# Optimization experiments

Measured on AMD Instinct MI355X. Metric: run time of the kernel, lower is better.

The kernel has to match this reference:

```python
import jax, jax.numpy as jnp
import numpy as np

L, B, S, D, H, E = 3, 2, 2048, 1024, 16, 4
Dh = D // H  # 64
DF = E * D   # 4096


def _ln(x, g, b, eps=1e-5):
    m = jnp.mean(x, axis=-1, keepdims=True)
    v = jnp.mean(jnp.square(x - m), axis=-1, keepdims=True)
    return (x - m) * jax.lax.rsqrt(v + eps) * g + b


def setup_inputs() -> dict:
    key = jax.random.key(0)
    ks = jax.random.split(key, 12)
    s = 0.02
    f32 = jnp.float32
    return {
        "x":    jax.random.normal(ks[0], (B, S, D), f32),
        "Wq":   jax.random.normal(ks[1], (L, Dh, Dh), f32) * s,
        "Wk":   jax.random.normal(ks[2], (L, Dh, Dh), f32) * s,
        "Wv":   jax.random.normal(ks[3], (L, Dh, Dh), f32) * s,
        "Wo":   jax.random.normal(ks[4], (L, D, D), f32) * s,
        "bo":   jnp.zeros((L, D), f32),
        "ln1_g": jnp.ones((L, D), f32),
        "ln1_b": jnp.zeros((L, D), f32),
        "W1":   jax.random.normal(ks[5], (L, DF, D), f32) * s,
        "b1":   jnp.zeros((L, DF), f32),
        "W2":   jax.random.normal(ks[6], (L, D, DF), f32) * s,
        "b2":   jnp.zeros((L, D), f32),
        "ln2_g": jnp.ones((L, D), f32),
        "ln2_b": jnp.zeros((L, D), f32),
    }


def reference(x, Wq, Wk, Wv, Wo, bo, ln1_g, ln1_b, W1, b1, W2, b2, ln2_g, ln2_b):
    scale = 1.0 / np.sqrt(Dh).astype(np.float32)
    out = x
    for l in range(L):
        xh = out.reshape(B, S, H, Dh)
        # per-head Linear (shared 64x64 weight across heads), torch Linear: y = x @ W.T
        q = jnp.einsum('bshd,ed->bhse', xh, Wq[l])  # [B,H,S,Dh]
        k = jnp.einsum('bshd,ed->bhse', xh, Wk[l])
        v = jnp.einsum('bshd,ed->bhse', xh, Wv[l])
        att = jax.nn.softmax(jnp.einsum('bhse,bhte->bhst', q, k) * scale, axis=-1)
        ctx = jnp.einsum('bhst,bhtd->bshd', att, v).reshape(B, S, D)
        att_out = ctx @ Wo[l].T + bo[l]
        n1 = _ln(att_out + out, ln1_g[l], ln1_b[l])  # residual adds layer input (v == out)
        ff = jax.nn.relu(n1 @ W1[l].T + b1[l]) @ W2[l].T + b2[l]
        out = _ln(ff + n1, ln2_g[l], ln2_b[l])
    return out
```

## Files before the change

kernel.cpp:

```cpp
#include <hip/hip_runtime.h>
#include <hip/hip_bf16.h>
#include <math.h>


#define DEVINL __device__ __forceinline__
typedef unsigned short ushort_t;
using short8 = __attribute__((ext_vector_type(8))) short;
using f32x4  = __attribute__((ext_vector_type(4))) float;

#if defined(__has_builtin)
#if __has_builtin(__builtin_amdgcn_exp2f)
#define EXPFN(x) __builtin_amdgcn_exp2f(x)
#define QSCALE 0.18033688011112042f
#define HAVE_EXP2 1
#endif
#endif
#ifndef HAVE_EXP2
#define EXPFN(x) __expf(x)
#define QSCALE 0.125f
#endif

DEVINL short f2b(float f) {
  unsigned u = __float_as_uint(f);
  u += 0x7fff + ((u >> 16) & 1);
  return (short)(u >> 16);
}
DEVINL unsigned pk2(float a, float b) {
  unsigned ua = __float_as_uint(a), ub = __float_as_uint(b);
  ua += 0x7fff + ((ua >> 16) & 1);
  ub += 0x7fff + ((ub >> 16) & 1);
  return (ua >> 16) | (ub & 0xffff0000u);
}
DEVINL unsigned pkc(float a, float b) {
  float2 f; f.x = a; f.y = b;
  __hip_bfloat162 h = __float22bfloat162_rn(f);
  return *reinterpret_cast<unsigned*>(&h);
}
DEVINL float bl(unsigned u) { return __uint_as_float(u << 16); }
DEVINL float bh(unsigned u) { return __uint_as_float(u & 0xffff0000u); }
DEVINL f32x4 mfma16(short8 a, short8 b, f32x4 c) {
  return __builtin_amdgcn_mfma_f32_16x16x32_bf16(a, b, c, 0, 0, 0);
}

typedef __attribute__((address_space(3))) void lds_void;
typedef __attribute__((address_space(1))) void gbl_void;
DEVINL void gl16(const void* g, void* l) {
  __builtin_amdgcn_global_load_lds((const gbl_void*)(unsigned long long)g,
                                   (lds_void*)(unsigned long long)l, 16, 0, 0);
}
template <int N> DEVINL void waitvm() {
  asm volatile("s_waitcnt vmcnt(%0)" ::"n"(N) : "memory");
}
DEVINL void barrier_raw() { __builtin_amdgcn_s_barrier(); }
DEVINL void sched0() { __builtin_amdgcn_sched_barrier(0); }

__global__ __launch_bounds__(256)
void conv_bf16(const float* __restrict__ src, ushort_t* __restrict__ dst,
               int n8) {
  int i = blockIdx.x * 256 + threadIdx.x;
  const int stride = gridDim.x * 256;
  for (; i < n8; i += stride) {
    float4 a = ((const float4*)src)[2 * i];
    float4 b = ((const float4*)src)[2 * i + 1];
    uint4 o;
    o.x = pk2(a.x, a.y); o.y = pk2(a.z, a.w);
    o.z = pk2(b.x, b.y); o.w = pk2(b.z, b.w);
    ((uint4*)dst)[i] = o;
  }
}

DEVINL float block_sum(float v, float* red) {
#pragma unroll
  for (int off = 32; off > 0; off >>= 1) v += __shfl_xor(v, off, 64);
  if ((threadIdx.x & 63) == 0) red[threadIdx.x >> 6] = v;
  __syncthreads();
  float r = red[0] + red[1] + red[2] + red[3];
  __syncthreads();
  return r;
}

template <bool WF>
__global__ __launch_bounds__(256)
void ln_fuse(const ushort_t* __restrict__ pa, const ushort_t* __restrict__ pb,
             const float* __restrict__ bias, const ushort_t* __restrict__ Rb,
             const float* __restrict__ g, const float* __restrict__ b,
             ushort_t* __restrict__ outb, float* __restrict__ outf) {
  __shared__ float red[4];
  const size_t base = (size_t)blockIdx.x * 1024 + threadIdx.x * 4;
  uint2 ua = *(const uint2*)(pa + base);
  uint2 ub = *(const uint2*)(pb + base);
  uint2 ur = *(const uint2*)(Rb + base);
  float4 vbi = *(const float4*)(bias + threadIdx.x * 4);
  float4 v;
  v.x = bl(ua.x) + bl(ub.x) + bl(ur.x) + vbi.x;
  v.y = bh(ua.x) + bh(ub.x) + bh(ur.x) + vbi.y;
  v.z = bl(ua.y) + bl(ub.y) + bl(ur.y) + vbi.z;
  v.w = bh(ua.y) + bh(ub.y) + bh(ur.y) + vbi.w;
  float s = block_sum(v.x + v.y + v.z + v.w, red);
  float mean = s * (1.0f / 1024.0f);
  float dx = v.x - mean, dy = v.y - mean, dz = v.z - mean, dw = v.w - mean;
  float sq = block_sum(dx * dx + dy * dy + dz * dz + dw * dw, red);
  float rstd = rsqrtf(sq * (1.0f / 1024.0f) + 1e-5f);
  const float4 gv = *(const float4*)(g + threadIdx.x * 4);
  const float4 bv = *(const float4*)(b + threadIdx.x * 4);
  float4 o;
  o.x = dx * rstd * gv.x + bv.x;
  o.y = dy * rstd * gv.y + bv.y;
  o.z = dz * rstd * gv.z + bv.z;
  o.w = dw * rstd * gv.w + bv.w;
  uint2 p;
  p.x = pk2(o.x, o.y); p.y = pk2(o.z, o.w);
  *(uint2*)(outb + base) = p;
  if (WF) *(float4*)(outf + base) = o;
}

template <int BM, int BN, int WR, int WC, bool OBF, int EPI, bool SWZ>
__global__ __launch_bounds__(WR * WC * 64)
void gemm_db(const ushort_t* __restrict__ A, const ushort_t* __restrict__ W,
             const float* __restrict__ bias, void* __restrict__ Cp, int M,
             int N, int Klen, int lda, int ldw) {
  constexpr int THREADS = WR * WC * 64;
  constexpr int FM = BM / WR / 16;
  constexpr int FN = BN / WC / 16;
  constexpr int CA = BM * 8 / THREADS;
  constexpr int CB = BN * 8 / THREADS;
  constexpr int L = CA + CB;
  __shared__ __align__(16) ushort_t As[2][BM * 64];
  __shared__ __align__(16) ushort_t Bs[2][BN * 64];
  const int tid = threadIdx.x;
  const int lane = tid & 63, lo = lane & 15, hi = lane >> 4, w = tid >> 6;
  int bx = blockIdx.x, by = blockIdx.y;
  if (SWZ) {
    int id = by * gridDim.x + bx;
    const int cpx = (gridDim.x * gridDim.y) >> 3;
    id = (id & 7) * cpx + (id >> 3);
    bx = id % gridDim.x;
    by = id / gridDim.x;
  }
  const int m0 = by * BM, n0 = bx * BN;
  const int wm = (w / WC) * (BM / WR), wn = (w % WC) * (BN / WC);
  const int kbase = blockIdx.z * Klen;

  auto stage = [&](int t, int buf) {
    const int k0 = kbase + t * 64;
#pragma unroll
    for (int i = 0; i < CA; ++i) {
      const int c = i * THREADS + tid;
      const int r = c >> 3, sg = (c & 7) ^ (r & 7);
      gl16(A + (size_t)(m0 + r) * lda + k0 + sg * 8, &As[buf][c * 8]);
    }
#pragma unroll
    for (int i = 0; i < CB; ++i) {
      const int c = i * THREADS + tid;
      const int r = c >> 3, sg = (c & 7) ^ (r & 7);
      gl16(W + (size_t)(n0 + r) * ldw + k0 + sg * 8, &Bs[buf][c * 8]);
    }
  };

  f32x4 acc[FM][FN] = {};
  auto compute = [&](int cur) {
#pragma unroll
    for (int ks = 0; ks < 2; ++ks) {
      short8 af[FM], bf_[FN];
#pragma unroll
      for (int fm = 0; fm < FM; ++fm) {
        const int row = wm + fm * 16 + lo;
        af[fm] = *(const short8*)
            &As[cur][row * 64 + (((ks * 4 + hi) ^ (row & 7)) << 3)];
      }
#pragma unroll
      for (int fn = 0; fn < FN; ++fn) {
        const int row = wn + fn * 16 + lo;
        bf_[fn] = *(const short8*)
            &Bs[cur][row * 64 + (((ks * 4 + hi) ^ (row & 7)) << 3)];
      }
#pragma unroll
      for (int fm = 0; fm < FM; ++fm)
#pragma unroll
        for (int fn = 0; fn < FN; ++fn)
          acc[fm][fn] = mfma16(af[fm], bf_[fn], acc[fm][fn]);
    }
  };

  const int nt = Klen / 64;
  stage(0, 0);
  for (int t = 0; t < nt - 1; ++t) {
    const int cur = t & 1;
    stage(t + 1, cur ^ 1);
    waitvm<L>();
    barrier_raw(); sched0();
    compute(cur);
    barrier_raw(); sched0();
  }
  waitvm<0>();
  barrier_raw(); sched0();
  compute((nt - 1) & 1);

  float bv[FN];
#pragma unroll
  for (int fn = 0; fn < FN; ++fn)
    bv[fn] = (EPI & 1) ? bias[n0 + wn + fn * 16 + lo] : 0.f;
#pragma unroll
  for (int fm = 0; fm < FM; ++fm)
#pragma unroll
    for (int fn = 0; fn < FN; ++fn) {
      const int col = n0 + wn + fn * 16 + lo;
#pragma unroll
      for (int r = 0; r < 4; ++r) {
        const int row = m0 + wm + fm * 16 + hi * 4 + r;
        float v = acc[fm][fn][r] + bv[fn];
        if (EPI & 4) v = fmaxf(v, 0.f);
        if (OBF) {
          ushort_t* Cb = (ushort_t*)Cp + (size_t)blockIdx.z * M * N;
          Cb[(size_t)row * N + col] = (ushort_t)f2b(v);
        } else {
          float* Cf = (float*)Cp + (size_t)blockIdx.z * M * N;
          Cf[(size_t)row * N + col] = v;
        }
      }
    }
}

__global__ __launch_bounds__(256)
void qkv_kernel(const ushort_t* __restrict__ A, const ushort_t* __restrict__ Wq,
                const ushort_t* __restrict__ Wk, const ushort_t* __restrict__ Wv,
                ushort_t* __restrict__ q, ushort_t* __restrict__ k,
                ushort_t* __restrict__ v) {
  __shared__ __align__(16) ushort_t As[128 * 64];
  __shared__ __align__(16) ushort_t Ws[3][64 * 64];
  const int tid = threadIdx.x;
  const int lane = tid & 63, lo = lane & 15, hi = lane >> 4, w = tid >> 6;
  const int m0 = blockIdx.x * 128;
  const int wm = (w >> 1) * 64, wn = (w & 1) * 32;

#pragma unroll
  for (int i = 0; i < 4; ++i) {
    const int c = i * 256 + tid;
    const int r = c >> 3, sg = (c & 7) ^ (r & 7);
    gl16(A + (size_t)(m0 + r) * 64 + sg * 8, As + c * 8);
  }
#pragma unroll
  for (int o = 0; o < 3; ++o) {
    const ushort_t* wb = (o == 0) ? Wq : (o == 1) ? Wk : Wv;
#pragma unroll
    for (int i = 0; i < 2; ++i) {
      const int c = i * 256 + tid;
      const int r = c >> 3, sg = (c & 7) ^ (r & 7);
      gl16(wb + (size_t)r * 64 + sg * 8, Ws[o] + c * 8);
    }
  }
  __syncthreads();

#pragma unroll
  for (int o = 0; o < 3; ++o) {
    ushort_t* ob = (o == 0) ? q : (o == 1) ? k : v;
    const float sc = (o == 0) ? QSCALE : 1.0f;
    f32x4 acc[4][2] = {};
#pragma unroll
    for (int ks = 0; ks < 2; ++ks) {
      short8 af[4], bf[2];
#pragma unroll
      for (int fm = 0; fm < 4; ++fm) {
        const int row = wm + fm * 16 + lo;
        af[fm] = *(const short8*)
            &As[row * 64 + (((ks * 4 + hi) ^ (row & 7)) << 3)];
      }
#pragma unroll
      for (int fn = 0; fn < 2; ++fn) {
        const int row = wn + fn * 16 + lo;
        bf[fn] = *(const short8*)
            &Ws[o][row * 64 + (((ks * 4 + hi) ^ (row & 7)) << 3)];
      }
#pragma unroll
      for (int fm = 0; fm < 4; ++fm)
#pragma unroll
        for (int fn = 0; fn < 2; ++fn)
          acc[fm][fn] = mfma16(af[fm], bf[fn], acc[fm][fn]);
    }
#pragma unroll
    for (int fm = 0; fm < 4; ++fm)
#pragma unroll
      for (int fn = 0; fn < 2; ++fn) {
        const int col = wn + fn * 16 + lo;
#pragma unroll
        for (int r = 0; r < 4; ++r) {
          const int row = m0 + wm + fm * 16 + hi * 4 + r;
          size_t idx;
          if (o == 2) {
            idx = (size_t)row * 64 + col;
          } else {
            idx = (size_t)((row >> 15) * 16 + (row & 15)) * 131072 +
                  (size_t)((row >> 4) & 2047) * 64 + col;
          }
          ob[idx] = (ushort_t)f2b(acc[fm][fn][r] * sc);
        }
      }
  }
}

__global__ __launch_bounds__(256)
void vtrans(const ushort_t* __restrict__ V, ushort_t* __restrict__ VT) {
  __shared__ ushort_t T[64][65];
  const int tid = threadIdx.x;
  const int s0 = blockIdx.x * 64, hd0 = blockIdx.y * 64, b = blockIdx.z;
  const ushort_t* src = V + (size_t)b * 2097152;
  ushort_t* dst = VT + (size_t)b * 2097152;
#pragma unroll
  for (int i = 0; i < 2; ++i) {
    int c = tid + i * 256;
    int s = c >> 3, kg = c & 7;
    short8 hv = *(const short8*)(src + (size_t)(s0 + s) * 1024 + hd0 + kg * 8);
#pragma unroll
    for (int j = 0; j < 8; ++j) T[s][kg * 8 + j] = (ushort_t)hv[j];
  }
  __syncthreads();
#pragma unroll
  for (int i = 0; i < 2; ++i) {
    int c = tid + i * 256;
    int hd = c >> 3, sg = c & 7;
    short8 o;
#pragma unroll
    for (int j = 0; j < 8; ++j) o[j] = (short)T[sg * 8 + j][hd];
    *(short8*)(dst + (size_t)(hd0 + hd) * 2048 + s0 + sg * 8) = o;
  }
}

__global__ __launch_bounds__(256)
void attn4(const ushort_t* __restrict__ Qh, const ushort_t* __restrict__ Kh,
           const ushort_t* __restrict__ VT, ushort_t* __restrict__ O) {
  __shared__ __align__(16) ushort_t Kbuf[2][64 * 64];
  __shared__ __align__(16) ushort_t Vbuf[2][64 * 64];
  __shared__ __align__(16) ushort_t Pbuf[4][2][16 * 40];
  const int tid = threadIdx.x, w = tid >> 6, lane = tid & 63;
  const int lo = lane & 15, hi = lane >> 4;
  const int hid = blockIdx.y * 16 + blockIdx.x;
  const int logical = (hid & 7) * 64 + (hid >> 3);
  const int bh = logical >> 4, qt = logical & 15;
  const int b = bh >> 4, h = bh & 15;
  const size_t hq = (size_t)bh * 131072;
  const size_t vth = (size_t)b * 2097152 + (size_t)h * 131072;
  const size_t oh = (size_t)b * 2097152 + (size_t)h * 64;
  const int qrow = qt * 128 + w * 32;
  ushort_t* Pa = Pbuf[w][0];
  ushort_t* Pb = Pbuf[w][1];

  const ushort_t* qpa = Qh + hq + (size_t)(qrow + lo) * 64 + hi * 8;
  const short8 qf0a = *(const short8*)qpa;
  const short8 qf1a = *(const short8*)(qpa + 32);
  const short8 qf0b = *(const short8*)(qpa + 1024);
  const short8 qf1b = *(const short8*)(qpa + 1024 + 32);

  const int c0 = tid, c1 = 256 + tid;
  const int r0 = c0 >> 3, s0 = ((c0 & 7) ^ (r0 & 7)) << 3;
  const int r1 = c1 >> 3, s1 = ((c1 & 7) ^ (r1 & 7)) << 3;
  const ushort_t* kg0 = Kh + hq + (size_t)r0 * 64 + s0;
  const ushort_t* kg1 = Kh + hq + (size_t)r1 * 64 + s1;
  const ushort_t* vg0 = VT + vth + (size_t)r0 * 2048 + s0;
  const ushort_t* vg1 = VT + vth + (size_t)r1 * 2048 + s1;

  auto stage = [&](int kt, int buf) {
    gl16(kg0 + (size_t)kt * 4096, &Kbuf[buf][c0 * 8]);
    gl16(kg1 + (size_t)kt * 4096, &Kbuf[buf][c1 * 8]);
    gl16(vg0 + kt * 64, &Vbuf[buf][c0 * 8]);
    gl16(vg1 + kt * 64, &Vbuf[buf][c1 * 8]);
  };

  f32x4 acca[4] = {}, accb[4] = {};
  f32x4 la = {}, lb = {};
  const int sw = lo & 7;
  const int ko0 = (hi ^ sw) << 3, ko1 = ((4 + hi) ^ sw) << 3;

  auto body = [&](const ushort_t* Kc, const ushort_t* Vc) {
    f32x4 sa[4], sb[4];
#pragma unroll
    for (int fm = 0; fm < 4; ++fm) {
      const int rb = (fm * 16 + lo) * 64;
      short8 k0 = *(const short8*)&Kc[rb + ko0];
      short8 k1 = *(const short8*)&Kc[rb + ko1];
      f32x4 ta = {};
      ta = mfma16(k0, qf0a, ta);
      ta = mfma16(k1, qf1a, ta);
      sa[fm] = ta;
      f32x4 tb = {};
      tb = mfma16(k0, qf0b, tb);
      tb = mfma16(k1, qf1b, tb);
      sb[fm] = tb;
    }
    short8 vf[4][2];
#pragma unroll
    for (int fn = 0; fn < 4; ++fn) {
      const int rb = (fn * 16 + lo) * 64;
      vf[fn][0] = *(const short8*)&Vc[rb + ko0];
      vf[fn][1] = *(const short8*)&Vc[rb + ko1];
    }
#pragma unroll
    for (int fm = 0; fm < 4; ++fm) {
      f32x4 p;
      p[0] = EXPFN(sa[fm][0]); p[1] = EXPFN(sa[fm][1]);
      p[2] = EXPFN(sa[fm][2]); p[3] = EXPFN(sa[fm][3]);
      la += p;
      uint2 pw;
      pw.x = pkc(p[0], p[1]); pw.y = pkc(p[2], p[3]);
      *(uint2*)&Pa[lo * 40 + fm * 16 + hi * 4] = pw;
      f32x4 r;
      r[0] = EXPFN(sb[fm][0]); r[1] = EXPFN(sb[fm][1]);
      r[2] = EXPFN(sb[fm][2]); r[3] = EXPFN(sb[fm][3]);
      lb += r;
      uint2 rw;
      rw.x = pkc(r[0], r[1]); rw.y = pkc(r[2], r[3]);
      *(uint2*)&Pb[lo * 40 + fm * 16 + hi * 4] = rw;
    }
    short8 pa0 = *(const short8*)&Pa[lo * 40 + hi * 8];
    short8 pa1 = *(const short8*)&Pa[lo * 40 + 32 + hi * 8];
    short8 pb0 = *(const short8*)&Pb[lo * 40 + hi * 8];
    short8 pb1 = *(const short8*)&Pb[lo * 40 + 32 + hi * 8];
#pragma unroll
    for (int fn = 0; fn < 4; ++fn) {
      acca[fn] = mfma16(vf[fn][0], pa0, acca[fn]);
      acca[fn] = mfma16(vf[fn][1], pa1, acca[fn]);
      accb[fn] = mfma16(vf[fn][0], pb0, accb[fn]);
      accb[fn] = mfma16(vf[fn][1], pb1, accb[fn]);
    }
  };

  stage(0, 0);
  __syncthreads();
  for (int kt2 = 0; kt2 < 16; ++kt2) {
    stage(2 * kt2 + 1, 1);
    body(Kbuf[0], Vbuf[0]);
    __syncthreads();
    if (kt2 < 15) stage(2 * kt2 + 2, 0);
    body(Kbuf[1], Vbuf[1]);
    __syncthreads();
  }

  float lsa = (la[0] + la[1]) + (la[2] + la[3]);
  lsa += __shfl_xor(lsa, 16);
  lsa += __shfl_xor(lsa, 32);
  float lsb = (lb[0] + lb[1]) + (lb[2] + lb[3]);
  lsb += __shfl_xor(lsb, 16);
  lsb += __shfl_xor(lsb, 32);
  const float inva = 1.0f / lsa, invb = 1.0f / lsb;
  ushort_t* opa = O + oh + (size_t)(qrow + lo) * 1024 + hi * 4;
  ushort_t* opb = opa + 16 * 1024;
#pragma unroll
  for (int fn = 0; fn < 4; ++fn) {
    uint2 oa, ob;
    oa.x = pk2(acca[fn][0] * inva, acca[fn][1] * inva);
    oa.y = pk2(acca[fn][2] * inva, acca[fn][3] * inva);
    ob.x = pk2(accb[fn][0] * invb, accb[fn][1] * invb);
    ob.y = pk2(accb[fn][2] * invb, accb[fn][3] * invb);
    *(uint2*)(opa + fn * 16) = oa;
    *(uint2*)(opb + fn * 16) = ob;
  }
}

extern "C" void kernel_launch(void* const* d_in, const int* in_sizes, int n_in,
                              void* d_out, int out_size, void* d_ws,
                              size_t ws_size, hipStream_t stream) {
  const float* x    = (const float*)d_in[0];
  const float* Wq   = (const float*)d_in[1];
  const float* Wk   = (const float*)d_in[2];
  const float* Wv   = (const float*)d_in[3];
  const float* Wo   = (const float*)d_in[4];
  const float* bo   = (const float*)d_in[5];
  const float* ln1g = (const float*)d_in[6];
  const float* ln1b = (const float*)d_in[7];
  const float* W1   = (const float*)d_in[8];
  const float* b1   = (const float*)d_in[9];
  const float* W2   = (const float*)d_in[10];
  const float* b2   = (const float*)d_in[11];
  const float* ln2g = (const float*)d_in[12];
  const float* ln2b = (const float*)d_in[13];
  float* out = (float*)d_out;
  char* wsb = (char*)d_ws;

  ushort_t* t0  = (ushort_t*)wsb;
  ushort_t* t0b = t0 + 4194304;
  ushort_t* q   = (ushort_t*)(wsb + (16ull << 20));
  ushort_t* k   = (ushort_t*)(wsb + (24ull << 20));
  ushort_t* v   = (ushort_t*)(wsb + (32ull << 20));
  ushort_t* vt  = (ushort_t*)(wsb + (40ull << 20));
  ushort_t* ff  = q;
  ushort_t* ctx = (ushort_t*)(wsb + (48ull << 20));
  ushort_t* n1b = ctx;
  ushort_t* xbf = (ushort_t*)(wsb + (56ull << 20));
  ushort_t* wqb = (ushort_t*)(wsb + (64ull << 20));
  ushort_t* wkb = wqb + 3 * 4096;
  ushort_t* wvb = wkb + 3 * 4096;
  ushort_t* wob = (ushort_t*)(wsb + (65ull << 20));
  ushort_t* w1b = (ushort_t*)(wsb + (72ull << 20));
  ushort_t* w2b = (ushort_t*)(wsb + (96ull << 20));

  auto conv = [&](const float* s, ushort_t* d, long n) {
    int n8 = (int)(n / 8);
    int g = (n8 + 255) / 256;
    if (g > 2048) g = 2048;
    conv_bf16<<<g, 256, 0, stream>>>(s, d, n8);
  };
  conv(x, xbf, 4194304);
  conv(Wq, wqb, 3 * 4096);
  conv(Wk, wkb, 3 * 4096);
  conv(Wv, wvb, 3 * 4096);
  conv(Wo, wob, 3ll * 1048576);
  conv(W1, w1b, 3ll * 4194304);
  conv(W2, w2b, 3ll * 4194304);

  const ushort_t* curb = xbf;
  for (int l = 0; l < 3; ++l) {
    qkv_kernel<<<512, 256, 0, stream>>>(curb, wqb + l * 4096, wkb + l * 4096,
                                        wvb + l * 4096, q, k, v);
    vtrans<<<dim3(32, 16, 2), 256, 0, stream>>>(v, vt);
    attn4<<<dim3(16, 32), 256, 0, stream>>>(q, k, vt, ctx);
    gemm_db<128, 128, 2, 2, true, 0, true>
        <<<dim3(8, 32, 2), 256, 0, stream>>>(ctx, wob + (size_t)l * 1048576,
                                             nullptr, t0, 4096, 1024, 512,
                                             1024, 1024);
    ln_fuse<false><<<4096, 256, 0, stream>>>(t0, t0b, bo + l * 1024, curb,
                                             ln1g + l * 1024, ln1b + l * 1024,
                                             n1b, nullptr);
    gemm_db<128, 128, 2, 2, true, 5, true>
        <<<dim3(32, 32, 1), 256, 0, stream>>>(n1b, w1b + (size_t)l * 4194304,
                                              b1 + l * 4096, ff, 4096, 4096,
                                              1024, 1024, 1024);
    gemm_db<128, 128, 2, 2, true, 0, true>
        <<<dim3(8, 32, 2), 256, 0, stream>>>(ff, w2b + (size_t)l * 4194304,
                                             nullptr, t0, 4096, 1024, 2048,
                                             4096, 4096);
    if (l == 2)
      ln_fuse<true><<<4096, 256, 0, stream>>>(t0, t0b, b2 + l * 1024, n1b,
                                              ln2g + l * 1024, ln2b + l * 1024,
                                              xbf, out);
    else
      ln_fuse<false><<<4096, 256, 0, stream>>>(t0, t0b, b2 + l * 1024, n1b,
                                               ln2g + l * 1024, ln2b + l * 1024,
                                               xbf, nullptr);
    curb = xbf;
  }
}
```

Measured before the change: 541.2 us.

## Use 256x256 eight-wave ping-pong GEMM for FFN up-projection

Adds a new GEMM kernel with 256x256 block tiles, 512 threads (8 waves), double-buffered LDS filled via global_load_lds, and a quadrant-interleaved schedule that alternates LDS reads, async stores and MFMA bursts with s_setprio. It also remaps block IDs to group neighbouring tiles for L2 reuse. It replaces the 128x128 gemm_db for the W1 GEMM (bias+ReLU epilogue). The larger tile raises arithmetic intensity, but it uses 128KB of LDS per block and the many barriers could limit overlap.

```diff
diff --git a/kernel.cpp b/kernel.cpp
--- a/kernel.cpp
+++ b/kernel.cpp
@@ -53,6 +53,9 @@
 }
 DEVINL void barrier_raw() { __builtin_amdgcn_s_barrier(); }
 DEVINL void sched0() { __builtin_amdgcn_sched_barrier(0); }
+DEVINL void waitlgkm0() {
+  asm volatile("s_waitcnt lgkmcnt(0)" ::: "memory");
+}
 
 __global__ __launch_bounds__(256)
 void conv_bf16(const float* __restrict__ src, ushort_t* __restrict__ dst,
@@ -221,6 +224,156 @@
     }
 }
 
+template <int EPI, bool SWZ>
+__global__ __launch_bounds__(512, 2)
+void gemm_8p(const ushort_t* __restrict__ A, const ushort_t* __restrict__ W,
+             const float* __restrict__ bias, ushort_t* __restrict__ Cp, int M,
+             int N, int K, int lda, int ldw) {
+  __shared__ __align__(16) ushort_t As[2][256 * 64];
+  __shared__ __align__(16) ushort_t Bs[2][256 * 64];
+  const int tid = threadIdx.x;
+  const int lane = tid & 63, lo = lane & 15, hi = lane >> 4, w = tid >> 6;
+  const int wr = w >> 2, wc = w & 3;
+  int bx = blockIdx.x, by = blockIdx.y;
+  if (SWZ) {
+    int id = by * gridDim.x + bx;
+    const int cpx = (gridDim.x * gridDim.y) >> 3;
+    id = (id & 7) * cpx + (id >> 3);
+    bx = id % gridDim.x;
+    by = id / gridDim.x;
+  }
+  const int m0 = by * 256, n0 = bx * 256;
+  const int wm = wr * 128, wn = wc * 64;
+
+  const int c0 = tid, c1 = 512 + tid;
+  const int r0 = c0 >> 3, g0 = ((c0 & 7) ^ (r0 & 7)) << 3;
+  const int r1 = c1 >> 3, g1 = ((c1 & 7) ^ (r1 & 7)) << 3;
+
+  auto stA = [&](int tile, int half, int buf) {
+    const ushort_t* s = A + (size_t)(m0 + half * 128) * lda + tile * 64;
+    ushort_t* d = &As[buf][half * 128 * 64];
+    gl16(s + (size_t)r0 * lda + g0, d + c0 * 8);
+    gl16(s + (size_t)r1 * lda + g1, d + c1 * 8);
+  };
+  auto stB = [&](int tile, int half, int buf) {
+    const ushort_t* s = W + (size_t)(n0 + half * 128) * ldw + tile * 64;
+    ushort_t* d = &Bs[buf][half * 128 * 64];
+    gl16(s + (size_t)r0 * ldw + g0, d + c0 * 8);
+    gl16(s + (size_t)r1 * ldw + g1, d + c1 * 8);
+  };
+
+  f32x4 acc[8][4] = {};
+  short8 af[2][4], bfA[2][2], bfB[2][2];
+
+  auto ldA = [&](int buf, int qr) {
+#pragma unroll
+    for (int ks = 0; ks < 2; ++ks)
+#pragma unroll
+      for (int fm = 0; fm < 4; ++fm) {
+        const int row = wm + qr * 64 + fm * 16 + lo;
+        af[ks][fm] = *(const short8*)
+            &As[buf][row * 64 + (((ks * 4 + hi) ^ (row & 7)) << 3)];
+      }
+  };
+  auto ldB = [&](int buf, int qc, short8 (&bf)[2][2]) {
+#pragma unroll
+    for (int ks = 0; ks < 2; ++ks)
+#pragma unroll
+      for (int fn = 0; fn < 2; ++fn) {
+        const int row = wn + qc * 32 + fn * 16 + lo;
+        bf[ks][fn] = *(const short8*)
+            &Bs[buf][row * 64 + (((ks * 4 + hi) ^ (row & 7)) << 3)];
+      }
+  };
+  auto mmaQ = [&](auto qr, auto qc, short8 (&bf)[2][2]) {
+    constexpr int QR = decltype(qr)::value, QC = decltype(qc)::value;
+    __builtin_amdgcn_s_setprio(1);
+#pragma unroll
+    for (int ks = 0; ks < 2; ++ks)
+#pragma unroll
+      for (int fm = 0; fm < 4; ++fm)
+#pragma unroll
+        for (int fn = 0; fn < 2; ++fn)
+          acc[QR * 4 + fm][QC * 2 + fn] = mfma16(
+              af[ks][fm], bf[ks][fn], acc[QR * 4 + fm][QC * 2 + fn]);
+    __builtin_amdgcn_s_setprio(0);
+  };
+  using I0 = std::integral_constant<int, 0>;
+  using I1 = std::integral_constant<int, 1>;
+
+  const int nt = K / 64;
+  const int ni = nt / 2;
+
+  stA(0, 0, 0); stA(0, 1, 0); stB(0, 0, 0); stB(0, 1, 0);
+  stB(1, 0, 1); stB(1, 1, 1);
+  waitvm<4>();
+  barrier_raw();
+
+  for (int j = 0; j < ni; ++j) {
+    const int t1 = 2 * j + 1, t2 = 2 * j + 2, t3 = 2 * j + 3;
+    const bool s2 = t2 < nt, s3 = t3 < nt;
+    const bool last = (j == ni - 1);
+    ldA(0, 0); ldB(0, 0, bfA);
+    stA(t1, 0, 1);
+    barrier_raw(); waitlgkm0(); sched0();
+    mmaQ(I0{}, I0{}, bfA);
+    barrier_raw();
+    ldB(0, 1, bfB);
+    stA(t1, 1, 1);
+    barrier_raw(); waitlgkm0(); sched0();
+    mmaQ(I0{}, I1{}, bfB);
+    barrier_raw();
+    ldA(0, 1);
+    if (s2) stB(t2, 0, 0);
+    barrier_raw(); waitlgkm0(); sched0();
+    mmaQ(I1{}, I1{}, bfB);
+    barrier_raw();
+    if (s2) stB(t2, 1, 0);
+    if (last) waitvm<0>(); else waitvm<4>();
+    barrier_raw();
+    mmaQ(I1{}, I0{}, bfA);
+    barrier_raw();
+    ldA(1, 0); ldB(1, 0, bfA);
+    if (s2) stA(t2, 0, 0);
+    barrier_raw(); waitlgkm0(); sched0();
+    mmaQ(I0{}, I0{}, bfA);
+    barrier_raw();
+    ldB(1, 1, bfB);
+    if (s2) stA(t2, 1, 0);
+    barrier_raw(); waitlgkm0(); sched0();
+    mmaQ(I0{}, I1{}, bfB);
+    barrier_raw();
+    ldA(1, 1);
+    if (s3) stB(t3, 0, 1);
+    barrier_raw(); waitlgkm0(); sched0();
+    mmaQ(I1{}, I1{}, bfB);
+    barrier_raw();
+    if (s3) stB(t3, 1, 1);
+    if (last) waitvm<0>(); else waitvm<4>();
+    barrier_raw();
+    mmaQ(I1{}, I0{}, bfA);
+    barrier_raw();
+  }
+
+  float bv[4];
+#pragma unroll
+  for (int fn = 0; fn < 4; ++fn)
+    bv[fn] = (EPI & 1) ? bias[n0 + wn + fn * 16 + lo] : 0.f;
+#pragma unroll
+  for (int fm = 0; fm < 8; ++fm)
+#pragma unroll
+    for (int fn = 0; fn < 4; ++fn) {
+      const int col = n0 + wn + fn * 16 + lo;
+#pragma unroll
+      for (int r = 0; r < 4; ++r) {
+        const int row = m0 + wm + fm * 16 + hi * 4 + r;
+        float v = acc[fm][fn][r] + bv[fn];
+        if (EPI & 4) v = fmaxf(v, 0.f);
+        Cp[(size_t)row * N + col] = (ushort_t)f2b(v);
+      }
+    }
+}
+
 __global__ __launch_bounds__(256)
 void qkv_kernel(const ushort_t* __restrict__ A, const ushort_t* __restrict__ Wq,
                 const ushort_t* __restrict__ Wk, const ushort_t* __restrict__ Wv,
@@ -519,10 +672,9 @@
     ln_fuse<false><<<4096, 256, 0, stream>>>(t0, t0b, bo + l * 1024, curb,
                                              ln1g + l * 1024, ln1b + l * 1024,
                                              n1b, nullptr);
-    gemm_db<128, 128, 2, 2, true, 5, true>
-        <<<dim3(32, 32, 1), 256, 0, stream>>>(n1b, w1b + (size_t)l * 4194304,
-                                              b1 + l * 4096, ff, 4096, 4096,
-                                              1024, 1024, 1024);
+    gemm_8p<5, true><<<dim3(16, 16), 512, 0, stream>>>(
+        n1b, w1b + (size_t)l * 4194304, b1 + l * 4096, ff, 4096, 4096, 1024,
+        1024, 1024);
     gemm_db<128, 128, 2, 2, true, 0, true>
         <<<dim3(8, 32, 2), 256, 0, stream>>>(ff, w2b + (size_t)l * 4194304,
                                              nullptr, t0, 4096, 1024, 2048,
```

After: 525.4 us. -2.9%, faster.
